# Optimization experiments

Hardware: AMD Instinct MI355X
Metric: run time of the kernel (lower is better)

## Reference

```python
import jax, jax.numpy as jnp
import numpy as np

D_MODEL = 1024
NUM_HEADS = 16
HEAD_DIM = D_MODEL // NUM_HEADS


def setup_inputs() -> dict:
    key = jax.random.key(0)
    ks = jax.random.split(key, 11)
    B, S, D = 2, 2048, D_MODEL
    s = 1.0 / np.sqrt(D)
    return {
        "query": jax.random.normal(ks[0], (B, S, D), jnp.float32),
        "key": jax.random.normal(ks[1], (B, S, D), jnp.float32),
        "value": jax.random.normal(ks[2], (B, S, D), jnp.float32),
        "W_q": jax.random.normal(ks[3], (D, D), jnp.float32) * s,
        "b_q": jnp.zeros((D,), jnp.float32),
        "W_k": jax.random.normal(ks[4], (D, D), jnp.float32) * s,
        "b_k": jnp.zeros((D,), jnp.float32),
        "W_v": jax.random.normal(ks[5], (D, D), jnp.float32) * s,
        "b_v": jnp.zeros((D,), jnp.float32),
        "W_o": jax.random.normal(ks[6], (D, D), jnp.float32) * s,
        "b_o": jnp.zeros((D,), jnp.float32),
    }


def reference(query, key, value, W_q, b_q, W_k, b_k, W_v, b_v, W_o, b_o):
    B, S, D = query.shape
    H, Dh = NUM_HEADS, HEAD_DIM
    # linear projections then split heads: [B, S, D] -> [B, H, S, Dh]
    def split_heads(x):
        return x.reshape(B, -1, H, Dh).transpose(0, 2, 1, 3)
    Q = split_heads(query @ W_q.T + b_q)
    K = split_heads(key @ W_k.T + b_k)
    V = split_heads(value @ W_v.T + b_v)
    # NOTE: original scales by d_model**-0.5, not head_dim**-0.5
    scale = jnp.asarray(D, Q.dtype) ** -0.5
    scores = jnp.einsum("bhqd,bhkd->bhqk", Q, K) * scale
    attn = jax.nn.softmax(scores, axis=-1)  # includes max-subtraction stabilization
    out = jnp.einsum("bhqk,bhkd->bhqd", attn, V)
    out = out.transpose(0, 2, 1, 3).reshape(B, -1, D)
    return out @ W_o.T + b_o
```

## Files before the change

kernel.cpp:

```cpp
#include <hip/hip_runtime.h>
#include <stdint.h>


typedef unsigned short u16;
typedef short s16x8 __attribute__((ext_vector_type(8)));
typedef short s16x4 __attribute__((ext_vector_type(4)));
typedef float f32x4 __attribute__((ext_vector_type(4)));
typedef u16 u16x4 __attribute__((ext_vector_type(4)));

#define S_LEN 2048
#define DMODEL 1024
#define LOG2E 1.44269504088896340736f

__device__ __forceinline__ u16 f2bf(float f) {
  union { float f; uint32_t u; } v; v.f = f;
  return (u16)((v.u + 0x8000u) >> 16);
}

__device__ __forceinline__ s16x8 ld8f(const float* s) {
  f32x4 a = *(const f32x4*)s;
  f32x4 b = *(const f32x4*)(s + 4);
  s16x8 r;
  r[0] = (short)f2bf(a[0]); r[1] = (short)f2bf(a[1]);
  r[2] = (short)f2bf(a[2]); r[3] = (short)f2bf(a[3]);
  r[4] = (short)f2bf(b[0]); r[5] = (short)f2bf(b[1]);
  r[6] = (short)f2bf(b[2]); r[7] = (short)f2bf(b[3]);
  return r;
}

__device__ __forceinline__ void gl2lds16(const u16* g, u16* l) {
  __builtin_amdgcn_global_load_lds(
      (const __attribute__((address_space(1))) uint32_t*)g,
      (__attribute__((address_space(3))) uint32_t*)l, 16, 0, 0);
}

struct Cvt7 { const float* s[7]; u16* d[7]; int n[7]; };

__global__ __launch_bounds__(256) void cvt7(Cvt7 p) {
  const int z = blockIdx.y;
  const int idx = blockIdx.x * 256 + threadIdx.x;
  if (idx * 8 < p.n[z])
    *(s16x8*)(p.d[z] + (size_t)idx * 8) = ld8f(p.s[z] + (size_t)idx * 8);
}

struct GemmBatch {
  const u16* A[3]; const u16* W[3]; const float* Bv[3]; void* C[3];
};

template <bool OUT_F32>
__global__ __launch_bounds__(256) void gemm_bt(GemmBatch p, int M, int N, int K) {
  __shared__ u16 As[128 * 64];
  __shared__ u16 Ws[128 * 64];
  const int z = blockIdx.z;
  const u16* __restrict__ A      = p.A[z];
  const u16* __restrict__ W      = p.W[z];
  const float* __restrict__ bias = p.Bv[z];

  const int tid = threadIdx.x;
  const int wave = tid >> 6, lane = tid & 63;
  const int quad = lane >> 4, l16 = lane & 15;
  const int bm = blockIdx.y * 128, bn = blockIdx.x * 128;
  const int wr = (wave >> 1) * 64, wc = (wave & 1) * 64;
  const int sr8 = lane >> 3;
  const int slc = (lane & 7) ^ sr8;
  const int srow = wave * 8 + sr8;

  f32x4 acc[4][4];
#pragma unroll
  for (int i = 0; i < 4; i++)
#pragma unroll
    for (int j = 0; j < 4; j++) acc[i][j] = {0.f, 0.f, 0.f, 0.f};

  const u16* Ab = A + (size_t)bm * K;
  const u16* Wb = W + (size_t)bn * K;

  for (int kt = 0; kt < K; kt += 64) {
    __syncthreads();
#pragma unroll
    for (int i = 0; i < 4; i++)
      gl2lds16(Ab + (size_t)(i * 32 + srow) * K + kt + slc * 8,
               &As[(i * 32 + wave * 8) * 64]);
#pragma unroll
    for (int i = 0; i < 4; i++)
      gl2lds16(Wb + (size_t)(i * 32 + srow) * K + kt + slc * 8,
               &Ws[(i * 32 + wave * 8) * 64]);
    __syncthreads();

#pragma unroll
    for (int ks = 0; ks < 2; ks++) {
      const int ch = ks * 4 + quad;
      s16x8 a[4], b[4];
#pragma unroll
      for (int t = 0; t < 4; t++)
        a[t] = *(const s16x8*)&As[(wr + t * 16 + l16) * 64 + ((ch ^ (l16 & 7)) << 3)];
#pragma unroll
      for (int t = 0; t < 4; t++)
        b[t] = *(const s16x8*)&Ws[(wc + t * 16 + l16) * 64 + ((ch ^ (l16 & 7)) << 3)];
#pragma unroll
      for (int i = 0; i < 4; i++)
#pragma unroll
        for (int j = 0; j < 4; j++)
          acc[i][j] = __builtin_amdgcn_mfma_f32_16x16x32_bf16(a[i], b[j], acc[i][j], 0, 0, 0);
    }
  }

#pragma unroll
  for (int j = 0; j < 4; j++) {
    const int col = bn + wc + j * 16 + l16;
    const float bv = bias[col];
#pragma unroll
    for (int i = 0; i < 4; i++) {
      const int row0 = bm + wr + i * 16 + quad * 4;
#pragma unroll
      for (int r = 0; r < 4; r++) {
        const float val = acc[i][j][r] + bv;
        if (OUT_F32)
          ((float*)p.C[z])[(size_t)(row0 + r) * N + col] = val;
        else
          ((u16*)p.C[z])[(size_t)(row0 + r) * N + col] = f2bf(val);
      }
    }
  }
}

__global__ __launch_bounds__(256) void transpose_v(const u16* __restrict__ Vp,
                                                   u16* __restrict__ Vt) {
  __shared__ u16 t[64 * 72];
  const int tid = threadIdx.x;
  const int bh = blockIdx.y, b = bh >> 4, h = bh & 15;
  const int s0 = blockIdx.x * 64;
  const int r = tid >> 4, c4 = (tid & 15) * 4;
#pragma unroll
  for (int i = 0; i < 4; i++) {
    const int s = i * 16 + r;
    u16x4 v = *(const u16x4*)&Vp[(size_t)(b * S_LEN + s0 + s) * DMODEL + h * 64 + c4];
    *(u16x4*)&t[s * 72 + c4] = v;
  }
  __syncthreads();
#pragma unroll
  for (int i = 0; i < 4; i++) {
    const int d = i * 16 + r;
    u16x4 v;
    v.x = t[(c4 + 0) * 72 + d];
    v.y = t[(c4 + 1) * 72 + d];
    v.z = t[(c4 + 2) * 72 + d];
    v.w = t[(c4 + 3) * 72 + d];
    *(u16x4*)&Vt[(size_t)(bh * 64 + d) * S_LEN + s0 + c4] = v;
  }
}

__global__ __launch_bounds__(256, 2) void attn_kernel(const u16* __restrict__ Qp,
                                                      const u16* __restrict__ Kp,
                                                      const u16* __restrict__ Vt,
                                                      u16* __restrict__ AO) {
  __shared__ u16 Qs[128 * 64];
  __shared__ u16 Ks[128 * 64];
  __shared__ u16 Vs[64 * 128];

  const int tid = threadIdx.x;
  const int wave = tid >> 6, lane = tid & 63;
  const int quad = lane >> 4, l16 = lane & 15;
  const int bh = blockIdx.y, b = bh >> 4, h = bh & 15;
  const int s0 = blockIdx.x * 128;
  const float c = 0.03125f * LOG2E;

  const int qr = lane >> 3, qc = lane & 7;
  const int vd = lane >> 4, vc = lane & 15;

#pragma unroll
  for (int i = 0; i < 4; i++) {
    const int rr = i * 32 + wave * 8 + qr;
    s16x8 qv = *(const s16x8*)(Qp + (size_t)(b * S_LEN + s0 + rr) * DMODEL + h * 64 + qc * 8);
    *(s16x8*)&Qs[rr * 64 + ((qc ^ qr) << 3)] = qv;
  }
  __syncthreads();

  s16x8 aq[2][2];
#pragma unroll
  for (int ks = 0; ks < 2; ks++)
#pragma unroll
    for (int rt = 0; rt < 2; rt++) {
      const int row = wave * 32 + rt * 16 + l16;
      const int ch = ks * 4 + quad;
      aq[ks][rt] = *(const s16x8*)&Qs[row * 64 + ((ch ^ (l16 & 7)) << 3)];
    }

  s16x8 kv[4], vv[4];
#pragma unroll
  for (int i = 0; i < 4; i++) {
    const int rr = i * 32 + wave * 8 + qr;
    kv[i] = *(const s16x8*)(Kp + (size_t)(b * S_LEN + rr) * DMODEL + h * 64 + qc * 8);
  }
#pragma unroll
  for (int i = 0; i < 4; i++) {
    const int dd = i * 16 + wave * 4 + vd;
    vv[i] = *(const s16x8*)(Vt + (size_t)(bh * 64 + dd) * S_LEN + vc * 8);
  }

  f32x4 o[2][4];
  float l_r[2] = {0.f, 0.f};
#pragma unroll
  for (int rt = 0; rt < 2; rt++)
#pragma unroll
    for (int dt = 0; dt < 4; dt++) o[rt][dt] = {0.f, 0.f, 0.f, 0.f};

  const f32x4 zf = {0.f, 0.f, 0.f, 0.f};

  for (int kt = 0; kt < S_LEN; kt += 128) {
    __syncthreads();
#pragma unroll
    for (int i = 0; i < 4; i++) {
      const int rr = i * 32 + wave * 8 + qr;
      *(s16x8*)&Ks[rr * 64 + ((qc ^ qr) << 3)] = kv[i];
    }
#pragma unroll
    for (int i = 0; i < 4; i++) {
      const int dd = i * 16 + wave * 4 + vd;
      *(s16x8*)&Vs[dd * 128 + ((vc ^ (dd & 15)) << 3)] = vv[i];
    }
    __syncthreads();

    if (kt + 128 < S_LEN) {
      const int k2 = kt + 128;
#pragma unroll
      for (int i = 0; i < 4; i++) {
        const int rr = i * 32 + wave * 8 + qr;
        kv[i] = *(const s16x8*)(Kp + (size_t)(b * S_LEN + k2 + rr) * DMODEL + h * 64 + qc * 8);
      }
#pragma unroll
      for (int i = 0; i < 4; i++) {
        const int dd = i * 16 + wave * 4 + vd;
        vv[i] = *(const s16x8*)(Vt + (size_t)(bh * 64 + dd) * S_LEN + k2 + vc * 8);
      }
    }

#pragma unroll
    for (int kvt = 0; kvt < 8; kvt++) {
      const int krow = kvt * 16 + l16;
      s16x8 ak0 = *(const s16x8*)&Ks[krow * 64 + (((0 + quad) ^ (l16 & 7)) << 3)];
      s16x8 ak1 = *(const s16x8*)&Ks[krow * 64 + (((4 + quad) ^ (l16 & 7)) << 3)];
      f32x4 sA, sB;
      sA = __builtin_amdgcn_mfma_f32_16x16x32_bf16(ak0, aq[0][0], zf, 0, 0, 0);
      sA = __builtin_amdgcn_mfma_f32_16x16x32_bf16(ak1, aq[1][0], sA, 0, 0, 0);
      sB = __builtin_amdgcn_mfma_f32_16x16x32_bf16(ak0, aq[0][1], zf, 0, 0, 0);
      sB = __builtin_amdgcn_mfma_f32_16x16x32_bf16(ak1, aq[1][1], sB, 0, 0, 0);

      s16x4 pf0, pf1;
      float rs0 = 0.f, rs1 = 0.f;
#pragma unroll
      for (int r = 0; r < 4; r++) {
        const float p0 = exp2f(sA[r] * c);
        const float p1 = exp2f(sB[r] * c);
        rs0 += p0; rs1 += p1;
        pf0[r] = (short)f2bf(p0);
        pf1[r] = (short)f2bf(p1);
      }
      l_r[0] += rs0; l_r[1] += rs1;

      const int ch = kvt * 2 + (quad >> 1);
#pragma unroll
      for (int dt = 0; dt < 4; dt++) {
        const int row = dt * 16 + l16;
        s16x4 bv = *(const s16x4*)&Vs[row * 128 + ((ch ^ l16) << 3) + (quad & 1) * 4];
        o[0][dt] = __builtin_amdgcn_mfma_f32_16x16x16bf16_1k(pf0, bv, o[0][dt], 0, 0, 0);
        o[1][dt] = __builtin_amdgcn_mfma_f32_16x16x16bf16_1k(pf1, bv, o[1][dt], 0, 0, 0);
      }
    }
  }

#pragma unroll
  for (int rt = 0; rt < 2; rt++) {
    l_r[rt] += __shfl_xor(l_r[rt], 16);
    l_r[rt] += __shfl_xor(l_r[rt], 32);
  }
#pragma unroll
  for (int rt = 0; rt < 2; rt++) {
#pragma unroll
    for (int r = 0; r < 4; r++) {
      const float linv = 1.f / __shfl(l_r[rt], quad * 4 + r);
      const int row = s0 + wave * 32 + rt * 16 + quad * 4 + r;
#pragma unroll
      for (int dt = 0; dt < 4; dt++)
        AO[(size_t)(b * S_LEN + row) * DMODEL + h * 64 + dt * 16 + l16] =
            f2bf(o[rt][dt][r] * linv);
    }
  }
}

extern "C" void kernel_launch(void* const* d_in, const int* in_sizes, int n_in,
                              void* d_out, int out_size, void* d_ws, size_t ws_size,
                              hipStream_t stream) {
  const float* query = (const float*)d_in[0];
  const float* key_  = (const float*)d_in[1];
  const float* value = (const float*)d_in[2];
  const float* W_q = (const float*)d_in[3];
  const float* b_q = (const float*)d_in[4];
  const float* W_k = (const float*)d_in[5];
  const float* b_k = (const float*)d_in[6];
  const float* W_v = (const float*)d_in[7];
  const float* b_v = (const float*)d_in[8];
  const float* W_o = (const float*)d_in[9];
  const float* b_o = (const float*)d_in[10];
  float* out = (float*)d_out;

  const int M = 2 * S_LEN;
  const int N = DMODEL, K = DMODEL;
  const size_t WSZ = (size_t)DMODEL * DMODEL;
  const size_t SZ  = (size_t)M * DMODEL;

  u16* Wqb = (u16*)d_ws;
  u16* Wkb = Wqb + WSZ;
  u16* Wvb = Wkb + WSZ;
  u16* Wob = Wvb + WSZ;
  u16* Qa  = Wob + WSZ;
  u16* Ka  = Qa + SZ;
  u16* Va  = Ka + SZ;
  u16* Qp  = Va + SZ;
  u16* Kp  = Qp + SZ;
  u16* Vp  = Kp + SZ;
  u16* Vt  = Qa;
  u16* AO  = Qp;

  Cvt7 cw;
  cw.s[0] = W_q;   cw.d[0] = Wqb; cw.n[0] = (int)WSZ;
  cw.s[1] = W_k;   cw.d[1] = Wkb; cw.n[1] = (int)WSZ;
  cw.s[2] = W_v;   cw.d[2] = Wvb; cw.n[2] = (int)WSZ;
  cw.s[3] = W_o;   cw.d[3] = Wob; cw.n[3] = (int)WSZ;
  cw.s[4] = query; cw.d[4] = Qa;  cw.n[4] = (int)SZ;
  cw.s[5] = key_;  cw.d[5] = Ka;  cw.n[5] = (int)SZ;
  cw.s[6] = value; cw.d[6] = Va;  cw.n[6] = (int)SZ;
  cvt7<<<dim3((int)(SZ / 2048), 7), 256, 0, stream>>>(cw);

  GemmBatch p1;
  p1.A[0] = Qa; p1.W[0] = Wqb; p1.Bv[0] = b_q; p1.C[0] = Qp;
  p1.A[1] = Ka; p1.W[1] = Wkb; p1.Bv[1] = b_k; p1.C[1] = Kp;
  p1.A[2] = Va; p1.W[2] = Wvb; p1.Bv[2] = b_v; p1.C[2] = Vp;
  gemm_bt<false><<<dim3(N / 128, M / 128, 3), 256, 0, stream>>>(p1, M, N, K);

  transpose_v<<<dim3(S_LEN / 64, 32), 256, 0, stream>>>(Vp, Vt);

  attn_kernel<<<dim3(S_LEN / 128, 32), 256, 0, stream>>>(Qp, Kp, Vt, AO);

  GemmBatch p2;
  p2.A[0] = AO; p2.W[0] = Wob; p2.Bv[0] = b_o; p2.C[0] = out;
  p2.A[1] = AO; p2.W[1] = Wob; p2.Bv[1] = b_o; p2.C[1] = out;
  p2.A[2] = AO; p2.W[2] = Wob; p2.Bv[2] = b_o; p2.C[2] = out;
  gemm_bt<true><<<dim3(N / 128, M / 128, 1), 256, 0, stream>>>(p2, M, N, K);
}
```

Baseline: 259.1 us.

## Double-buffer GEMM LDS tiles and fuse V transpose into attention

The projection GEMM now uses two LDS buffers with a K-step of 32. Each iteration prefetches the next tile into the alternate buffer while computing the current one, leaving one barrier per iteration instead of two. The separate transpose_v kernel is removed: attention loads V rows directly and scatters them transposed into LDS with scalar 16-bit stores. This saves a kernel launch and a global round trip for V, at the cost of many narrow LDS writes in the attention loop.

```diff
diff --git a/kernel.cpp b/kernel.cpp
--- a/kernel.cpp
+++ b/kernel.cpp
@@ -6,7 +6,6 @@
 typedef short s16x8 __attribute__((ext_vector_type(8)));
 typedef short s16x4 __attribute__((ext_vector_type(4)));
 typedef float f32x4 __attribute__((ext_vector_type(4)));
-typedef u16 u16x4 __attribute__((ext_vector_type(4)));
 
 #define S_LEN 2048
 #define DMODEL 1024
@@ -49,8 +48,8 @@
 
 template <bool OUT_F32>
 __global__ __launch_bounds__(256) void gemm_bt(GemmBatch p, int M, int N, int K) {
-  __shared__ u16 As[128 * 64];
-  __shared__ u16 Ws[128 * 64];
+  __shared__ u16 As[2][64 * 64];
+  __shared__ u16 Ws[2][64 * 64];
   const int z = blockIdx.z;
   const u16* __restrict__ A      = p.A[z];
   const u16* __restrict__ W      = p.W[z];
@@ -61,9 +60,20 @@
   const int quad = lane >> 4, l16 = lane & 15;
   const int bm = blockIdx.y * 128, bn = blockIdx.x * 128;
   const int wr = (wave >> 1) * 64, wc = (wave & 1) * 64;
-  const int sr8 = lane >> 3;
-  const int slc = (lane & 7) ^ sr8;
-  const int srow = wave * 8 + sr8;
+  const int ha = wr >> 6, hb = wc >> 6;
+
+  const int pr8 = lane >> 3;
+  const int pc  = lane & 7;
+  const int lc  = pc ^ pr8;
+  const int hh  = lc >> 2;
+  const int kc  = lc & 3;
+
+  size_t goff[2];
+#pragma unroll
+  for (int i = 0; i < 2; i++) {
+    const int prow = wave * 16 + i * 8 + pr8;
+    goff[i] = (size_t)(hh * 64 + prow) * K + kc * 8;
+  }
 
   f32x4 acc[4][4];
 #pragma unroll
@@ -74,34 +84,39 @@
   const u16* Ab = A + (size_t)bm * K;
   const u16* Wb = W + (size_t)bn * K;
 
-  for (int kt = 0; kt < K; kt += 64) {
+#pragma unroll
+  for (int i = 0; i < 2; i++) {
+    gl2lds16(Ab + goff[i], &As[0][(wave * 16 + i * 8) * 64]);
+    gl2lds16(Wb + goff[i], &Ws[0][(wave * 16 + i * 8) * 64]);
+  }
+
+  const int NIT = K / 32;
+  for (int it = 0; it < NIT; it++) {
+    const int cur = it & 1;
     __syncthreads();
+    if (it + 1 < NIT) {
+      const int kt2 = (it + 1) * 32;
+#pragma unroll
+      for (int i = 0; i < 2; i++) {
+        gl2lds16(Ab + goff[i] + kt2, &As[cur ^ 1][(wave * 16 + i * 8) * 64]);
+        gl2lds16(Wb + goff[i] + kt2, &Ws[cur ^ 1][(wave * 16 + i * 8) * 64]);
+      }
+    }
+
+    s16x8 a[4], b[4];
+#pragma unroll
+    for (int t = 0; t < 4; t++)
+      a[t] = *(const s16x8*)&As[cur][(t * 16 + l16) * 64 +
+                                     (((ha * 4 + quad) ^ (l16 & 7)) << 3)];
+#pragma unroll
+    for (int t = 0; t < 4; t++)
+      b[t] = *(const s16x8*)&Ws[cur][(t * 16 + l16) * 64 +
+                                     (((hb * 4 + quad) ^ (l16 & 7)) << 3)];
 #pragma unroll
     for (int i = 0; i < 4; i++)
-      gl2lds16(Ab + (size_t)(i * 32 + srow) * K + kt + slc * 8,
-               &As[(i * 32 + wave * 8) * 64]);
-#pragma unroll
-    for (int i = 0; i < 4; i++)
-      gl2lds16(Wb + (size_t)(i * 32 + srow) * K + kt + slc * 8,
-               &Ws[(i * 32 + wave * 8) * 64]);
-    __syncthreads();
-
-#pragma unroll
-    for (int ks = 0; ks < 2; ks++) {
-      const int ch = ks * 4 + quad;
-      s16x8 a[4], b[4];
-#pragma unroll
-      for (int t = 0; t < 4; t++)
-        a[t] = *(const s16x8*)&As[(wr + t * 16 + l16) * 64 + ((ch ^ (l16 & 7)) << 3)];
-#pragma unroll
-      for (int t = 0; t < 4; t++)
-        b[t] = *(const s16x8*)&Ws[(wc + t * 16 + l16) * 64 + ((ch ^ (l16 & 7)) << 3)];
-#pragma unroll
-      for (int i = 0; i < 4; i++)
-#pragma unroll
-        for (int j = 0; j < 4; j++)
-          acc[i][j] = __builtin_amdgcn_mfma_f32_16x16x32_bf16(a[i], b[j], acc[i][j], 0, 0, 0);
-    }
+#pragma unroll
+      for (int j = 0; j < 4; j++)
+        acc[i][j] = __builtin_amdgcn_mfma_f32_16x16x32_bf16(a[i], b[j], acc[i][j], 0, 0, 0);
   }
 
 #pragma unroll
@@ -123,35 +138,9 @@
   }
 }
 
-__global__ __launch_bounds__(256) void transpose_v(const u16* __restrict__ Vp,
-                                                   u16* __restrict__ Vt) {
-  __shared__ u16 t[64 * 72];
-  const int tid = threadIdx.x;
-  const int bh = blockIdx.y, b = bh >> 4, h = bh & 15;
-  const int s0 = blockIdx.x * 64;
-  const int r = tid >> 4, c4 = (tid & 15) * 4;
-#pragma unroll
-  for (int i = 0; i < 4; i++) {
-    const int s = i * 16 + r;
-    u16x4 v = *(const u16x4*)&Vp[(size_t)(b * S_LEN + s0 + s) * DMODEL + h * 64 + c4];
-    *(u16x4*)&t[s * 72 + c4] = v;
-  }
-  __syncthreads();
-#pragma unroll
-  for (int i = 0; i < 4; i++) {
-    const int d = i * 16 + r;
-    u16x4 v;
-    v.x = t[(c4 + 0) * 72 + d];
-    v.y = t[(c4 + 1) * 72 + d];
-    v.z = t[(c4 + 2) * 72 + d];
-    v.w = t[(c4 + 3) * 72 + d];
-    *(u16x4*)&Vt[(size_t)(bh * 64 + d) * S_LEN + s0 + c4] = v;
-  }
-}
-
 __global__ __launch_bounds__(256, 2) void attn_kernel(const u16* __restrict__ Qp,
                                                       const u16* __restrict__ Kp,
-                                                      const u16* __restrict__ Vt,
+                                                      const u16* __restrict__ Vp,
                                                       u16* __restrict__ AO) {
   __shared__ u16 Qs[128 * 64];
   __shared__ u16 Ks[128 * 64];
@@ -165,7 +154,6 @@
   const float c = 0.03125f * LOG2E;
 
   const int qr = lane >> 3, qc = lane & 7;
-  const int vd = lane >> 4, vc = lane & 15;
 
 #pragma unroll
   for (int i = 0; i < 4; i++) {
@@ -190,11 +178,7 @@
   for (int i = 0; i < 4; i++) {
     const int rr = i * 32 + wave * 8 + qr;
     kv[i] = *(const s16x8*)(Kp + (size_t)(b * S_LEN + rr) * DMODEL + h * 64 + qc * 8);
-  }
-#pragma unroll
-  for (int i = 0; i < 4; i++) {
-    const int dd = i * 16 + wave * 4 + vd;
-    vv[i] = *(const s16x8*)(Vt + (size_t)(bh * 64 + dd) * S_LEN + vc * 8);
+    vv[i] = *(const s16x8*)(Vp + (size_t)(b * S_LEN + rr) * DMODEL + h * 64 + qc * 8);
   }
 
   f32x4 o[2][4];
@@ -215,8 +199,12 @@
     }
 #pragma unroll
     for (int i = 0; i < 4; i++) {
-      const int dd = i * 16 + wave * 4 + vd;
-      *(s16x8*)&Vs[dd * 128 + ((vc ^ (dd & 15)) << 3)] = vv[i];
+      const int cch = i * 4 + wave;
+#pragma unroll
+      for (int j = 0; j < 8; j++) {
+        const int d = qc * 8 + j;
+        Vs[d * 128 + ((cch ^ (d & 15)) << 3) + qr] = (u16)vv[i][j];
+      }
     }
     __syncthreads();
 
@@ -226,11 +214,7 @@
       for (int i = 0; i < 4; i++) {
         const int rr = i * 32 + wave * 8 + qr;
         kv[i] = *(const s16x8*)(Kp + (size_t)(b * S_LEN + k2 + rr) * DMODEL + h * 64 + qc * 8);
-      }
-#pragma unroll
-      for (int i = 0; i < 4; i++) {
-        const int dd = i * 16 + wave * 4 + vd;
-        vv[i] = *(const s16x8*)(Vt + (size_t)(bh * 64 + dd) * S_LEN + k2 + vc * 8);
+        vv[i] = *(const s16x8*)(Vp + (size_t)(b * S_LEN + k2 + rr) * DMODEL + h * 64 + qc * 8);
       }
     }
 
@@ -318,7 +302,6 @@
   u16* Qp  = Va + SZ;
   u16* Kp  = Qp + SZ;
   u16* Vp  = Kp + SZ;
-  u16* Vt  = Qa;
   u16* AO  = Qp;
 
   Cvt7 cw;
@@ -337,9 +320,7 @@
   p1.A[2] = Va; p1.W[2] = Wvb; p1.Bv[2] = b_v; p1.C[2] = Vp;
   gemm_bt<false><<<dim3(N / 128, M / 128, 3), 256, 0, stream>>>(p1, M, N, K);
 
-  transpose_v<<<dim3(S_LEN / 64, 32), 256, 0, stream>>>(Vp, Vt);
-
-  attn_kernel<<<dim3(S_LEN / 128, 32), 256, 0, stream>>>(Qp, Kp, Vt, AO);
+  attn_kernel<<<dim3(S_LEN / 128, 32), 256, 0, stream>>>(Qp, Kp, Vp, AO);
 
   GemmBatch p2;
   p2.A[0] = AO; p2.W[0] = Wob; p2.Bv[0] = b_o; p2.C[0] = out;
```

New measurement: 269.6 us. 4.0% more time.
